# Performance work log

Measured on AMD Instinct MI355X. Metric: run time of the kernel, lower is better.

Reference implementation:

```python
import jax, jax.numpy as jnp
import numpy as np

N_WORDS, MAX_CHARS = 32768, 16
WORD_DIM, CHAR_DIM, HIDDEN = 256, 64, 256
VOCAB = 256


def setup_inputs() -> dict:
    key = jax.random.key(0)
    ks = jax.random.split(key, 10)
    char_indices = jax.random.randint(ks[0], (N_WORDS, MAX_CHARS), 0, VOCAB)
    char_lengths = jax.random.randint(ks[1], (N_WORDS,), 1, MAX_CHARS + 1)
    word_emb = jax.random.normal(ks[2], (N_WORDS, WORD_DIM), dtype=jnp.float32)
    s = 0.05
    E_char = jax.random.normal(ks[3], (VOCAB, CHAR_DIM), dtype=jnp.float32) * s
    W_ih = jax.random.normal(ks[4], (4 * HIDDEN, CHAR_DIM), dtype=jnp.float32) * s
    W_hh = jax.random.normal(ks[5], (4 * HIDDEN, HIDDEN), dtype=jnp.float32) * s
    b_ih = jax.random.normal(ks[6], (4 * HIDDEN,), dtype=jnp.float32) * s
    b_hh = jax.random.normal(ks[7], (4 * HIDDEN,), dtype=jnp.float32) * s
    W_lin = jax.random.normal(ks[8], (WORD_DIM, WORD_DIM + HIDDEN), dtype=jnp.float32) * s
    b_lin = jax.random.normal(ks[9], (WORD_DIM,), dtype=jnp.float32) * s
    return dict(char_indices=char_indices, char_lengths=char_lengths,
                word_emb=word_emb, E_char=E_char, W_ih=W_ih, W_hh=W_hh,
                b_ih=b_ih, b_hh=b_hh, W_lin=W_lin, b_lin=b_lin)


def _lstm_last_hidden(x, lengths, W_ih, W_hh, b_ih, b_hh):
    # x: [N, T, E]; returns final hidden h at position length-1 per row.
    N, T, _ = x.shape
    H = W_hh.shape[1]
    x_proj = jnp.einsum('nte,ge->ntg', x, W_ih) + (b_ih + b_hh)  # [N, T, 4H]
    x_proj = jnp.transpose(x_proj, (1, 0, 2))                    # time-major [T, N, 4H]

    def step(carry, inp):
        h, c = carry
        xg, t = inp
        gates = xg + h @ W_hh.T
        i, f, g, o = jnp.split(gates, 4, axis=-1)
        i, f, o = jax.nn.sigmoid(i), jax.nn.sigmoid(f), jax.nn.sigmoid(o)
        g = jnp.tanh(g)
        c_new = f * c + i * g
        h_new = o * jnp.tanh(c_new)
        mask = (t < lengths)[:, None]  # freeze state past each word's length
        h = jnp.where(mask, h_new, h)
        c = jnp.where(mask, c_new, c)
        return (h, c), None

    h0 = jnp.zeros((N, H), dtype=x.dtype)
    c0 = jnp.zeros((N, H), dtype=x.dtype)
    (h, _), _ = jax.lax.scan(step, (h0, c0), (x_proj, jnp.arange(T)))
    return h


def reference(char_indices, char_lengths, word_emb, E_char, W_ih, W_hh,
              b_ih, b_hh, W_lin, b_lin):
    char_embedded = E_char[char_indices]                        # [N, T, E]
    h = _lstm_last_hidden(char_embedded, char_lengths, W_ih, W_hh, b_ih, b_hh)
    combined = jnp.concatenate([word_emb, h], axis=-1)          # [N, WORD+H]
    return jax.nn.relu(combined @ W_lin.T + b_lin)              # [N, WORD]
```

## Files before the change

kernel.cpp:

```cpp
#include <hip/hip_runtime.h>


#define NW 32768

typedef __attribute__((ext_vector_type(8))) short short8;
typedef __attribute__((ext_vector_type(4))) float f32x4;
typedef __attribute__((ext_vector_type(4))) int i32x4;

#define MFMA16(a,b,c) __builtin_amdgcn_mfma_f32_16x16x32_bf16(a,b,c,0,0,0)
#define MFMAI8(a,b,c) __builtin_amdgcn_mfma_i32_16x16x32_i8(a,b,c,0,0,0)

#define O_ORDER 0
#define O_SLEN  131072
#define O_WPK   262144
#define O_USTP  589824
#define O_BIAS  593920
#define O_CHT   598016
#define O_WLIN  614400

__device__ inline unsigned short f2b(float f) {
  unsigned u = __builtin_bit_cast(unsigned, f);
  u = u + 0x7fffu + ((u >> 16) & 1u);
  return (unsigned short)(u >> 16);
}
__device__ inline float fsigm(float x) {
  float e = __builtin_amdgcn_exp2f(-1.44269504f * x);
  return __builtin_amdgcn_rcpf(1.0f + e);
}
__device__ inline float ftanh(float x) {
  float e = __builtin_amdgcn_exp2f(2.88539008f * x);
  return 1.0f - 2.0f * __builtin_amdgcn_rcpf(e + 1.0f);
}

__global__ void k_prep0(const float* __restrict__ wih, const float* __restrict__ whh,
                        const float* __restrict__ bih, const float* __restrict__ bhh,
                        const float* __restrict__ ech, unsigned char* __restrict__ ws) {
  int i = blockIdx.x * 256 + threadIdx.x;
  if (i < 1024) {
    float mx = 0.f;
    for (int k = 0; k < 64; ++k)  mx = fmaxf(mx, fabsf(wih[i * 64 + k]) * 0.25f);
    for (int k = 0; k < 256; ++k) mx = fmaxf(mx, fabsf(whh[i * 256 + k]));
    ((float*)(ws + O_USTP))[i] = mx / (127.f * 127.f);
    ((float*)(ws + O_BIAS))[i] = bih[i] + bhh[i];
    return;
  }
  int j = i - 1024;
  if (j < 16384) {
    float v = 508.f * ech[j];
    int q = (int)__builtin_rintf(v);
    q = q < -127 ? -127 : (q > 127 ? 127 : q);
    ((signed char*)(ws + O_CHT))[j] = (signed char)q;
  }
}

__global__ void k_prep1(const float* __restrict__ wih, const float* __restrict__ whh,
                        const float* __restrict__ wlin, unsigned char* __restrict__ ws) {
  int i = blockIdx.x * 256 + threadIdx.x;
  if (i < 327680) {
    int j = i & 7, lane = (i >> 3) & 63, t2 = i >> 9;
    int nt = t2 & 7, u2 = t2 >> 3;
    int kb = u2 % 10, w = u2 / 10;
    int n = (nt >> 1) * 256 + w * 32 + (nt & 1) * 16 + (lane & 15);
    int k = kb * 32 + (lane >> 4) * 8 + j;
    float v = (k < 64) ? wih[n * 64 + k] * 0.25f : whh[n * 256 + (k - 64)];
    float ustep = ((const float*)(ws + O_USTP))[n] * 127.f;
    float qf = (ustep > 0.f) ? v / ustep : 0.f;
    int q = (int)__builtin_rintf(qf);
    q = q < -127 ? -127 : (q > 127 ? 127 : q);
    ((signed char*)(ws + O_WPK))[i] = (signed char)q;
    return;
  }
  int i2 = i - 327680;
  if (i2 < 131072) {
    int j = i2 & 7, lane = (i2 >> 3) & 63, t3 = i2 >> 9;
    int kf = t3 & 15, nn = t3 >> 4;
    int n = (nn >> 2) * 64 + (nn & 3) * 16 + (lane & 15);
    int k = kf * 32 + (lane >> 4) * 8 + j;
    ((unsigned short*)(ws + O_WLIN))[i2] = f2b(wlin[n * 512 + k]);
  }
}

__global__ void k_sort(const int* __restrict__ lens, unsigned char* __restrict__ ws) {
  __shared__ unsigned hist[16], pos[16];
  int tid = threadIdx.x;
  if (tid < 16) hist[tid] = 0;
  __syncthreads();
  for (int w = tid; w < NW; w += 1024) {
    int l = lens[w]; l = l < 1 ? 1 : (l > 16 ? 16 : l);
    atomicAdd(&hist[l - 1], 1u);
  }
  __syncthreads();
  if (tid == 0) {
    unsigned acc = 0;
    for (int l = 0; l < 16; ++l) { pos[l] = acc; acc += hist[l]; }
  }
  __syncthreads();
  int* order = (int*)(ws + O_ORDER);
  int* slenp = (int*)(ws + O_SLEN);
  for (int w = tid; w < NW; w += 1024) {
    int l = lens[w]; l = l < 1 ? 1 : (l > 16 ? 16 : l);
    unsigned p = atomicAdd(&pos[l - 1], 1u);
    order[p] = w; slenp[p] = l;
  }
}

__global__ __launch_bounds__(512, 2) void k_main(
    const int* __restrict__ cidx, const float* __restrict__ wemb,
    const float* __restrict__ blin, float* __restrict__ outp,
    const unsigned char* __restrict__ ws) {
  extern __shared__ signed char smem[];
  signed char (*WL)[8][8][64][8] = (signed char (*)[8][8][64][8])smem;
  signed char (*Xb)[10][64][8] = (signed char (*)[10][64][8])(smem + 98304);
  signed char (*CT)[64] = (signed char (*)[64])(smem + 98304 + 20480);
  int (*CW)[16] = (int (*)[16])(smem + 98304 + 20480 + 16384);

  const int tid = threadIdx.x, b = blockIdx.x;
  const int w = tid >> 6, lane = tid & 63;
  const int q = lane >> 4, l15 = lane & 15;

  const int* order = (const int*)(ws + O_ORDER);
  const int* slen  = (const int*)(ws + O_SLEN);
  const signed char* wpk = (const signed char*)(ws + O_WPK);
  const float* upt = (const float*)(ws + O_USTP);
  const float* bsg = (const float*)(ws + O_BIAS);
  const unsigned short* wlin = (const unsigned short*)(ws + O_WLIN);

  {
    long* d = (long*)&CT[0][0];
    const long* s = (const long*)(ws + O_CHT);
    #pragma unroll
    for (int ii = 0; ii < 4; ++ii) d[tid + 512 * ii] = s[tid + 512 * ii];
  }
  long wreg[7][8];
  #pragma unroll
  for (int kb = 0; kb < 7; ++kb)
    #pragma unroll
    for (int nt = 0; nt < 8; ++nt)
      wreg[kb][nt] = *(const long*)(wpk + (((w * 10 + kb) * 8 + nt) * 64 + lane) * 8);
  #pragma unroll
  for (int c = 0; c < 24; ++c) {
    int kb = c >> 3, nt = c & 7;
    *(long*)&WL[kb][w][nt][lane][0] =
        *(const long*)(wpk + (((w * 10 + 7 + kb) * 8 + nt) * 64 + lane) * 8);
  }
  float uq[8], bq[8];
  #pragma unroll
  for (int nt = 0; nt < 8; ++nt) {
    int n = (nt >> 1) * 256 + w * 32 + (nt & 1) * 16 + l15;
    uq[nt] = upt[n]; bq[nt] = bsg[n];
  }
  const int mh = w >> 2, nw = w & 3;
  float blv[4];
  #pragma unroll
  for (int nt = 0; nt < 4; ++nt) blv[nt] = blin[nw * 64 + nt * 16 + l15];

  for (int sl = 0; sl < 2; ++sl) {
    const int s = sl ? (511 - b) : b;
    const int base = 64 * s;
    __syncthreads();

    {
      long* p = (long*)&Xb[0][0][0][0];
      #pragma unroll
      for (int ii = 0; ii < 4; ++ii) {
        int idx = tid + 512 * ii;
        int mt = idx >> 9, rem = idx & 511;
        p[mt * 640 + 128 + rem] = 0L;
      }
    }
    if (tid < 256) {
      int m = tid >> 2, part = tid & 3;
      int wid = order[base + m];
      *(i32x4*)&CW[m][part * 4] = *(const i32x4*)(cidx + wid * 16 + part * 4);
    }
    int tmax[4]; unsigned lenpk[4];
    #pragma unroll
    for (int mt = 0; mt < 4; ++mt) {
      int pbm = base + 16 * mt;
      tmax[mt] = slen[pbm + 15];
      unsigned l0 = (unsigned)slen[pbm + q * 4 + 0];
      unsigned l1 = (unsigned)slen[pbm + q * 4 + 1];
      unsigned l2 = (unsigned)slen[pbm + q * 4 + 2];
      unsigned l3 = (unsigned)slen[pbm + q * 4 + 3];
      lenpk[mt] = l0 | (l1 << 8) | (l2 << 16) | (l3 << 24);
    }
    const int Tm = tmax[3];
    __syncthreads();
    {
      int m = tid >> 3, c = tid & 7, kb = c >> 2, kq = c & 3;
      int ch = CW[m][0] & 255;
      *(long*)&Xb[m >> 4][kb][(m & 15) + 16 * kq][0] = *(const long*)&CT[ch][kb * 32 + kq * 8];
    }
    __syncthreads();

    float creg[4][2][4];
    #pragma unroll
    for (int mt = 0; mt < 4; ++mt)
      #pragma unroll
      for (int hs = 0; hs < 2; ++hs)
        #pragma unroll
        for (int r = 0; r < 4; ++r) creg[mt][hs][r] = 0.f;
    unsigned hpack[4][2];

    for (int t = 0; t < Tm; ++t) {
      bool actm[4];
      actm[0] = t < tmax[0]; actm[1] = t < tmax[1];
      actm[2] = t < tmax[2]; actm[3] = true;

      #pragma unroll
      for (int mt = 0; mt < 4; ++mt) {
        if (!actm[mt]) continue;
        i32x4 acc[8];
        #pragma unroll
        for (int nt = 0; nt < 8; ++nt) acc[nt] = (i32x4)0;
        #pragma unroll
        for (int kb = 0; kb < 7; ++kb) {
          long A = *(const long*)&Xb[mt][kb][lane][0];
          #pragma unroll
          for (int nt = 0; nt < 8; ++nt) acc[nt] = MFMAI8(A, wreg[kb][nt], acc[nt]);
        }
        #pragma unroll
        for (int kb = 7; kb < 10; ++kb) {
          long A = *(const long*)&Xb[mt][kb][lane][0];
          #pragma unroll
          for (int nt = 0; nt < 8; ++nt) {
            long Bv = *(const long*)&WL[kb - 7][w][nt][lane][0];
            acc[nt] = MFMAI8(A, Bv, acc[nt]);
          }
        }
        #pragma unroll
        for (int hs = 0; hs < 2; ++hs) {
          unsigned hp = 0;
          #pragma unroll
          for (int r = 0; r < 4; ++r) {
            float gi = (float)acc[0 + hs][r] * uq[0 + hs] + bq[0 + hs];
            float gf = (float)acc[2 + hs][r] * uq[2 + hs] + bq[2 + hs];
            float gg = (float)acc[4 + hs][r] * uq[4 + hs] + bq[4 + hs];
            float go = (float)acc[6 + hs][r] * uq[6 + hs] + bq[6 + hs];
            float si = fsigm(gi), sf = fsigm(gf);
            float sg = ftanh(gg), so = fsigm(go);
            float cold = creg[mt][hs][r];
            float cn = sf * cold + si * sg;
            float hn = so * ftanh(cn);
            int lene = (int)((lenpk[mt] >> (8 * r)) & 255u);
            creg[mt][hs][r] = (t < lene) ? cn : cold;
            int hq = (int)__builtin_rintf(127.f * hn);
            hq = hq < -127 ? -127 : (hq > 127 ? 127 : hq);
            hp |= ((unsigned)hq & 255u) << (8 * r);
          }
          hpack[mt][hs] = hp;
        }
      }
      __syncthreads();

      #pragma unroll
      for (int mt = 0; mt < 4; ++mt) {
        if (!actm[mt]) continue;
        #pragma unroll
        for (int hs = 0; hs < 2; ++hs) {
          int kqp = hs * 2 + (l15 >> 3);
          #pragma unroll
          for (int r = 0; r < 4; ++r) {
            int lene = (int)((lenpk[mt] >> (8 * r)) & 255u);
            if (t < lene)
              Xb[mt][2 + w][(q * 4 + r) + 16 * kqp][l15 & 7] =
                  (signed char)((hpack[mt][hs] >> (8 * r)) & 255u);
          }
        }
      }
      if (t + 1 < Tm) {
        int m = tid >> 3, c = tid & 7, kb = c >> 2, kq = c & 3;
        int ch = CW[m][t + 1] & 255;
        *(long*)&Xb[m >> 4][kb][(m & 15) + 16 * kq][0] = *(const long*)&CT[ch][kb * 32 + kq * 8];
      }
      __syncthreads();
    }

    int widA[2];
    #pragma unroll
    for (int mi = 0; mi < 2; ++mi) widA[mi] = order[base + (2 * mh + mi) * 16 + l15];
    f32x4 fac[2][4];
    #pragma unroll
    for (int mi = 0; mi < 2; ++mi)
      #pragma unroll
      for (int nt = 0; nt < 4; ++nt) fac[mi][nt] = 0.0f;

    #pragma unroll
    for (int kf = 0; kf < 16; ++kf) {
      short8 Bn[4];
      #pragma unroll
      for (int nt = 0; nt < 4; ++nt)
        Bn[nt] = ((const short8*)wlin)[((nw * 4 + nt) * 16 + kf) * 64 + lane];
      short8 Am[2];
      #pragma unroll
      for (int mi = 0; mi < 2; ++mi) {
        if (kf < 8) {
          const f32x4* pa = (const f32x4*)(wemb + widA[mi] * 256 + kf * 32 + q * 8);
          f32x4 f0 = pa[0], f1 = pa[1];
          short8 A;
          A[0] = (short)f2b(f0[0]); A[1] = (short)f2b(f0[1]);
          A[2] = (short)f2b(f0[2]); A[3] = (short)f2b(f0[3]);
          A[4] = (short)f2b(f1[0]); A[5] = (short)f2b(f1[1]);
          A[6] = (short)f2b(f1[2]); A[7] = (short)f2b(f1[3]);
          Am[mi] = A;
        } else {
          long ch = *(const long*)&Xb[2 * mh + mi][kf - 6][lane][0];
          short8 A;
          #pragma unroll
          for (int j = 0; j < 8; ++j) {
            int v = (int)(signed char)((ch >> (8 * j)) & 255);
            A[j] = (short)f2b((float)v * (1.f / 127.f));
          }
          Am[mi] = A;
        }
      }
      #pragma unroll
      for (int mi = 0; mi < 2; ++mi)
        #pragma unroll
        for (int nt = 0; nt < 4; ++nt)
          fac[mi][nt] = MFMA16(Am[mi], Bn[nt], fac[mi][nt]);
    }
    #pragma unroll
    for (int mi = 0; mi < 2; ++mi) {
      #pragma unroll
      for (int r = 0; r < 4; ++r) {
        int wid = order[base + (2 * mh + mi) * 16 + q * 4 + r];
        float* po = outp + wid * 256 + nw * 64 + l15;
        #pragma unroll
        for (int nt = 0; nt < 4; ++nt) {
          float v = fac[mi][nt][r] + blv[nt];
          po[nt * 16] = v > 0.f ? v : 0.f;
        }
      }
    }
  }
}

extern "C" void kernel_launch(void* const* d_in, const int* in_sizes, int n_in,
                              void* d_out, int out_size, void* d_ws, size_t ws_size,
                              hipStream_t stream) {
  const int*   cidx = (const int*)d_in[0];
  const int*   clen = (const int*)d_in[1];
  const float* wemb = (const float*)d_in[2];
  const float* ech  = (const float*)d_in[3];
  const float* wih  = (const float*)d_in[4];
  const float* whh  = (const float*)d_in[5];
  const float* bih  = (const float*)d_in[6];
  const float* bhh  = (const float*)d_in[7];
  const float* wlin = (const float*)d_in[8];
  const float* blin = (const float*)d_in[9];
  float* outp = (float*)d_out;
  unsigned char* ws = (unsigned char*)d_ws;

  k_prep0<<<68, 256, 0, stream>>>(wih, whh, bih, bhh, ech, ws);
  k_prep1<<<1792, 256, 0, stream>>>(wih, whh, wlin, ws);
  k_sort<<<1, 1024, 0, stream>>>(clen, ws);
  k_main<<<256, 512, 139264, stream>>>(cidx, wemb, blin, outp, ws);
}
```

Baseline: 449.7 us.

## Use 16x16x64 int8 MFMA, double-buffer LSTM state, and overlap MFMA with gate math

Measured after the change: 740.1 us. 1.65x slower.

```diff
diff --git a/kernel.cpp b/kernel.cpp
--- a/kernel.cpp
+++ b/kernel.cpp
@@ -7,8 +7,8 @@
 typedef __attribute__((ext_vector_type(4))) float f32x4;
 typedef __attribute__((ext_vector_type(4))) int i32x4;
 
-#define MFMA16(a,b,c) __builtin_amdgcn_mfma_f32_16x16x32_bf16(a,b,c,0,0,0)
-#define MFMAI8(a,b,c) __builtin_amdgcn_mfma_i32_16x16x32_i8(a,b,c,0,0,0)
+#define MFMA16(a,b,c)  __builtin_amdgcn_mfma_f32_16x16x32_bf16(a,b,c,0,0,0)
+#define MFMAI64(a,b,c) __builtin_amdgcn_mfma_i32_16x16x64_i8(a,b,c,0,0,0)
 
 #define O_ORDER 0
 #define O_SLEN  131072
@@ -23,45 +23,40 @@
   u = u + 0x7fffu + ((u >> 16) & 1u);
   return (unsigned short)(u >> 16);
 }
-__device__ inline float fsigm(float x) {
-  float e = __builtin_amdgcn_exp2f(-1.44269504f * x);
-  return __builtin_amdgcn_rcpf(1.0f + e);
-}
-__device__ inline float ftanh(float x) {
-  float e = __builtin_amdgcn_exp2f(2.88539008f * x);
-  return 1.0f - 2.0f * __builtin_amdgcn_rcpf(e + 1.0f);
-}
-
-__global__ void k_prep0(const float* __restrict__ wih, const float* __restrict__ whh,
+
+__global__ void k_prepA(const float* __restrict__ wih, const float* __restrict__ whh,
                         const float* __restrict__ bih, const float* __restrict__ bhh,
                         const float* __restrict__ ech, unsigned char* __restrict__ ws) {
-  int i = blockIdx.x * 256 + threadIdx.x;
-  if (i < 1024) {
-    float mx = 0.f;
-    for (int k = 0; k < 64; ++k)  mx = fmaxf(mx, fabsf(wih[i * 64 + k]) * 0.25f);
-    for (int k = 0; k < 256; ++k) mx = fmaxf(mx, fabsf(whh[i * 256 + k]));
-    ((float*)(ws + O_USTP))[i] = mx / (127.f * 127.f);
-    ((float*)(ws + O_BIAS))[i] = bih[i] + bhh[i];
+  int b = blockIdx.x, tid = threadIdx.x;
+  if (b < 256) {
+    int n = b * 4 + (tid >> 6), lane = tid & 63;
+    float m = fabsf(wih[n * 64 + lane]) * 0.25f;
+    #pragma unroll
+    for (int c = 0; c < 4; ++c) m = fmaxf(m, fabsf(whh[n * 256 + c * 64 + lane]));
+    #pragma unroll
+    for (int off = 32; off; off >>= 1) m = fmaxf(m, __shfl_xor(m, off));
+    if (lane == 0) {
+      ((float*)(ws + O_USTP))[n] = m / 16129.f;
+      ((float*)(ws + O_BIAS))[n] = bih[n] + bhh[n];
+    }
     return;
   }
-  int j = i - 1024;
-  if (j < 16384) {
-    float v = 508.f * ech[j];
-    int q = (int)__builtin_rintf(v);
-    q = q < -127 ? -127 : (q > 127 ? 127 : q);
-    ((signed char*)(ws + O_CHT))[j] = (signed char)q;
-  }
-}
-
-__global__ void k_prep1(const float* __restrict__ wih, const float* __restrict__ whh,
+  int idx = (b - 256) * 256 + tid;
+  int q = (int)__builtin_rintf(508.f * ech[idx]);
+  q = q < -127 ? -127 : (q > 127 ? 127 : q);
+  ((signed char*)(ws + O_CHT))[idx] = (signed char)q;
+}
+
+__global__ void k_prepB(const float* __restrict__ wih, const float* __restrict__ whh,
                         const float* __restrict__ wlin, unsigned char* __restrict__ ws) {
   int i = blockIdx.x * 256 + threadIdx.x;
   if (i < 327680) {
-    int j = i & 7, lane = (i >> 3) & 63, t2 = i >> 9;
-    int nt = t2 & 7, u2 = t2 >> 3;
-    int kb = u2 % 10, w = u2 / 10;
-    int n = (nt >> 1) * 256 + w * 32 + (nt & 1) * 16 + (lane & 15);
-    int k = kb * 32 + (lane >> 4) * 8 + j;
+    int j = i & 15, lane = (i >> 4) & 63, t = i >> 10;
+    int f = t & 7, u = t >> 3;
+    int kb = u % 5, w = u / 5;
+    int g = f >> 1, cc = f & 1;
+    int n = g * 256 + w * 32 + cc * 16 + (lane & 15);
+    int k = kb * 64 + (lane >> 4) * 16 + j;
     float v = (k < 64) ? wih[n * 64 + k] * 0.25f : whh[n * 256 + (k - 64)];
     float ustep = ((const float*)(ws + O_USTP))[n] * 127.f;
     float qf = (ustep > 0.f) ? v / ustep : 0.f;
@@ -71,13 +66,11 @@
     return;
   }
   int i2 = i - 327680;
-  if (i2 < 131072) {
-    int j = i2 & 7, lane = (i2 >> 3) & 63, t3 = i2 >> 9;
-    int kf = t3 & 15, nn = t3 >> 4;
-    int n = (nn >> 2) * 64 + (nn & 3) * 16 + (lane & 15);
-    int k = kf * 32 + (lane >> 4) * 8 + j;
-    ((unsigned short*)(ws + O_WLIN))[i2] = f2b(wlin[n * 512 + k]);
-  }
+  int j = i2 & 7, lane = (i2 >> 3) & 63, t3 = i2 >> 9;
+  int kf = t3 & 15, nn = t3 >> 4;
+  int n = (nn >> 2) * 64 + (nn & 3) * 16 + (lane & 15);
+  int k = kf * 32 + (lane >> 4) * 8 + j;
+  ((unsigned short*)(ws + O_WLIN))[i2] = f2b(wlin[n * 512 + k]);
 }
 
 __global__ void k_sort(const int* __restrict__ lens, unsigned char* __restrict__ ws) {
@@ -104,15 +97,19 @@
   }
 }
 
+#define L_WL 40960
+#define L_CT 106496
+#define L_CW 122880
+
 __global__ __launch_bounds__(512, 2) void k_main(
     const int* __restrict__ cidx, const float* __restrict__ wemb,
     const float* __restrict__ blin, float* __restrict__ outp,
     const unsigned char* __restrict__ ws) {
-  extern __shared__ signed char smem[];
-  signed char (*WL)[8][8][64][8] = (signed char (*)[8][8][64][8])smem;
-  signed char (*Xb)[10][64][8] = (signed char (*)[10][64][8])(smem + 98304);
-  signed char (*CT)[64] = (signed char (*)[64])(smem + 98304 + 20480);
-  int (*CW)[16] = (int (*)[16])(smem + 98304 + 20480 + 16384);
+  extern __shared__ unsigned char smem[];
+  signed char (*Xb)[4][5][64][16] = (signed char (*)[4][5][64][16])smem;
+  signed char (*WL)[8][64][16]    = (signed char (*)[8][64][16])(smem + L_WL);
+  signed char (*CT)[64]           = (signed char (*)[64])(smem + L_CT);
+  int (*CW)[16]                   = (int (*)[16])(smem + L_CW);
 
   const int tid = threadIdx.x, b = blockIdx.x;
   const int w = tid >> 6, lane = tid & 63;
@@ -121,34 +118,29 @@
   const int* order = (const int*)(ws + O_ORDER);
   const int* slen  = (const int*)(ws + O_SLEN);
   const signed char* wpk = (const signed char*)(ws + O_WPK);
-  const float* upt = (const float*)(ws + O_USTP);
-  const float* bsg = (const float*)(ws + O_BIAS);
   const unsigned short* wlin = (const unsigned short*)(ws + O_WLIN);
 
-  {
-    long* d = (long*)&CT[0][0];
-    const long* s = (const long*)(ws + O_CHT);
-    #pragma unroll
-    for (int ii = 0; ii < 4; ++ii) d[tid + 512 * ii] = s[tid + 512 * ii];
-  }
-  long wreg[7][8];
+  ((i32x4*)CT)[tid]       = ((const i32x4*)(ws + O_CHT))[tid];
+  ((i32x4*)CT)[512 + tid] = ((const i32x4*)(ws + O_CHT))[512 + tid];
+  i32x4 wreg[4][8];
   #pragma unroll
-  for (int kb = 0; kb < 7; ++kb)
-    #pragma unroll
-    for (int nt = 0; nt < 8; ++nt)
-      wreg[kb][nt] = *(const long*)(wpk + (((w * 10 + kb) * 8 + nt) * 64 + lane) * 8);
+  for (int kb = 0; kb < 4; ++kb)
+    #pragma unroll
+    for (int f = 0; f < 8; ++f)
+      wreg[kb][f] = *(const i32x4*)(wpk + (((w * 5 + kb) * 8 + f) * 64 + lane) * 16);
   #pragma unroll
-  for (int c = 0; c < 24; ++c) {
-    int kb = c >> 3, nt = c & 7;
-    *(long*)&WL[kb][w][nt][lane][0] =
-        *(const long*)(wpk + (((w * 10 + 7 + kb) * 8 + nt) * 64 + lane) * 8);
-  }
-  float uq[8], bq[8];
+  for (int f = 0; f < 8; ++f)
+    *(i32x4*)&WL[w][f][lane][0] =
+        *(const i32x4*)(wpk + (((w * 5 + 4) * 8 + f) * 64 + lane) * 16);
+  float uq[2][4], bq[2][4];
   #pragma unroll
-  for (int nt = 0; nt < 8; ++nt) {
-    int n = (nt >> 1) * 256 + w * 32 + (nt & 1) * 16 + l15;
-    uq[nt] = upt[n]; bq[nt] = bsg[n];
-  }
+  for (int cc = 0; cc < 2; ++cc)
+    #pragma unroll
+    for (int g = 0; g < 4; ++g) {
+      int n = g * 256 + w * 32 + cc * 16 + l15;
+      uq[cc][g] = ((const float*)(ws + O_USTP))[n];
+      bq[cc][g] = ((const float*)(ws + O_BIAS))[n];
+    }
   const int mh = w >> 2, nw = w & 3;
   float blv[4];
   #pragma unroll
@@ -160,12 +152,11 @@
     __syncthreads();
 
     {
-      long* p = (long*)&Xb[0][0][0][0];
-      #pragma unroll
-      for (int ii = 0; ii < 4; ++ii) {
+      #pragma unroll
+      for (int ii = 0; ii < 2; ++ii) {
         int idx = tid + 512 * ii;
-        int mt = idx >> 9, rem = idx & 511;
-        p[mt * 640 + 128 + rem] = 0L;
+        int mt = idx >> 8, off = idx & 255;
+        *(i32x4*)(&Xb[0][mt][1][0][0] + off * 16) = (i32x4)0;
       }
     }
     if (tid < 256) {
@@ -173,109 +164,108 @@
       int wid = order[base + m];
       *(i32x4*)&CW[m][part * 4] = *(const i32x4*)(cidx + wid * 16 + part * 4);
     }
-    int tmax[4]; unsigned lenpk[4];
+    unsigned lenpk[4];
     #pragma unroll
     for (int mt = 0; mt < 4; ++mt) {
       int pbm = base + 16 * mt;
-      tmax[mt] = slen[pbm + 15];
       unsigned l0 = (unsigned)slen[pbm + q * 4 + 0];
       unsigned l1 = (unsigned)slen[pbm + q * 4 + 1];
       unsigned l2 = (unsigned)slen[pbm + q * 4 + 2];
       unsigned l3 = (unsigned)slen[pbm + q * 4 + 3];
       lenpk[mt] = l0 | (l1 << 8) | (l2 << 16) | (l3 << 24);
     }
-    const int Tm = tmax[3];
+    const int Tm = slen[base + 63];
     __syncthreads();
-    {
-      int m = tid >> 3, c = tid & 7, kb = c >> 2, kq = c & 3;
+    if (tid < 256) {
+      int m = tid >> 2, c = tid & 3;
       int ch = CW[m][0] & 255;
-      *(long*)&Xb[m >> 4][kb][(m & 15) + 16 * kq][0] = *(const long*)&CT[ch][kb * 32 + kq * 8];
+      *(i32x4*)&Xb[0][m >> 4][0][(m & 15) + 16 * c][0] = *(const i32x4*)&CT[ch][c * 16];
     }
     __syncthreads();
 
-    float creg[4][2][4];
+    f32x4 creg[4][2];
     #pragma unroll
     for (int mt = 0; mt < 4; ++mt)
       #pragma unroll
-      for (int hs = 0; hs < 2; ++hs)
-        #pragma unroll
-        for (int r = 0; r < 4; ++r) creg[mt][hs][r] = 0.f;
-    unsigned hpack[4][2];
+      for (int cc = 0; cc < 2; ++cc) creg[mt][cc] = 0.0f;
+    unsigned fhold[4][2] = {};
 
     for (int t = 0; t < Tm; ++t) {
-      bool actm[4];
-      actm[0] = t < tmax[0]; actm[1] = t < tmax[1];
-      actm[2] = t < tmax[2]; actm[3] = true;
-
-      #pragma unroll
-      for (int mt = 0; mt < 4; ++mt) {
-        if (!actm[mt]) continue;
-        i32x4 acc[8];
-        #pragma unroll
-        for (int nt = 0; nt < 8; ++nt) acc[nt] = (i32x4)0;
-        #pragma unroll
-        for (int kb = 0; kb < 7; ++kb) {
-          long A = *(const long*)&Xb[mt][kb][lane][0];
-          #pragma unroll
-          for (int nt = 0; nt < 8; ++nt) acc[nt] = MFMAI8(A, wreg[kb][nt], acc[nt]);
-        }
-        #pragma unroll
-        for (int kb = 7; kb < 10; ++kb) {
-          long A = *(const long*)&Xb[mt][kb][lane][0];
-          #pragma unroll
-          for (int nt = 0; nt < 8; ++nt) {
-            long Bv = *(const long*)&WL[kb - 7][w][nt][lane][0];
-            acc[nt] = MFMAI8(A, Bv, acc[nt]);
+      const int cur = t & 1, nxt = cur ^ 1;
+      i32x4 acc0[4], acc1[4];
+
+      auto stage_mfma = [&](int mt, int cc, i32x4* acc) {
+        #pragma unroll
+        for (int g = 0; g < 4; ++g) acc[g] = (i32x4)0;
+        #pragma unroll
+        for (int kb = 0; kb < 5; ++kb) {
+          i32x4 A = *(const i32x4*)&Xb[cur][mt][kb][lane][0];
+          if (kb < 4) {
+            #pragma unroll
+            for (int g = 0; g < 4; ++g)
+              acc[g] = MFMAI64(A, wreg[kb][g * 2 + cc], acc[g]);
+          } else {
+            #pragma unroll
+            for (int g = 0; g < 4; ++g) {
+              i32x4 Bv = *(const i32x4*)&WL[w][g * 2 + cc][lane][0];
+              acc[g] = MFMAI64(A, Bv, acc[g]);
+            }
           }
         }
-        #pragma unroll
-        for (int hs = 0; hs < 2; ++hs) {
-          unsigned hp = 0;
-          #pragma unroll
-          for (int r = 0; r < 4; ++r) {
-            float gi = (float)acc[0 + hs][r] * uq[0 + hs] + bq[0 + hs];
-            float gf = (float)acc[2 + hs][r] * uq[2 + hs] + bq[2 + hs];
-            float gg = (float)acc[4 + hs][r] * uq[4 + hs] + bq[4 + hs];
-            float go = (float)acc[6 + hs][r] * uq[6 + hs] + bq[6 + hs];
-            float si = fsigm(gi), sf = fsigm(gf);
-            float sg = ftanh(gg), so = fsigm(go);
-            float cold = creg[mt][hs][r];
-            float cn = sf * cold + si * sg;
-            float hn = so * ftanh(cn);
-            int lene = (int)((lenpk[mt] >> (8 * r)) & 255u);
-            creg[mt][hs][r] = (t < lene) ? cn : cold;
-            int hq = (int)__builtin_rintf(127.f * hn);
-            hq = hq < -127 ? -127 : (hq > 127 ? 127 : hq);
-            hp |= ((unsigned)hq & 255u) << (8 * r);
-          }
-          hpack[mt][hs] = hp;
+      };
+      auto stage_update = [&](int mt, int cc, i32x4* acc) {
+        const int kbh = 1 + ((w * 2 + cc) >> 2);
+        const int sub = (4 + w * 2 + cc) & 3;
+        unsigned fh = fhold[mt][cc], newf = 0;
+        #pragma unroll
+        for (int r = 0; r < 4; ++r) {
+          float gi = (float)acc[0][r] * uq[cc][0] + bq[cc][0];
+          float gf = (float)acc[1][r] * uq[cc][1] + bq[cc][1];
+          float gg = (float)acc[2][r] * uq[cc][2] + bq[cc][2];
+          float go = (float)acc[3][r] * uq[cc][3] + bq[cc][3];
+          gi = fminf(30.f, fmaxf(-30.f, gi));
+          gf = fminf(30.f, fmaxf(-30.f, gf));
+          gg = fminf(30.f, fmaxf(-30.f, gg));
+          go = fminf(30.f, fmaxf(-30.f, go));
+          float ei  = __builtin_amdgcn_exp2f(-1.44269504f * gi);
+          float ef  = __builtin_amdgcn_exp2f(-1.44269504f * gf);
+          float eg2 = __builtin_amdgcn_exp2f( 2.88539008f * gg);
+          float eo  = __builtin_amdgcn_exp2f(-1.44269504f * go);
+          float cold = creg[mt][cc][r];
+          float cn = cold * __builtin_amdgcn_rcpf(1.f + ef) +
+                     (eg2 - 1.f) * __builtin_amdgcn_rcpf((1.f + ei) * (1.f + eg2));
+          float ec = __builtin_amdgcn_exp2f(2.88539008f * cn);
+          float hn = (ec - 1.f) * __builtin_amdgcn_rcpf((1.f + eo) * (ec + 1.f));
+          int lene = (int)((lenpk[mt] >> (8 * r)) & 255u);
+          bool act = t < lene;
+          creg[mt][cc][r] = act ? cn : cold;
+          int hq = (int)__builtin_rintf(127.f * hn);
+          hq = hq < -127 ? -127 : (hq > 127 ? 127 : hq);
+          unsigned ob = act ? ((unsigned)hq & 255u) : ((fh >> (8 * r)) & 255u);
+          newf |= ob << (8 * r);
+          if (t <= lene)
+            Xb[nxt][mt][kbh][(q * 4 + r) + 16 * sub][l15] = (signed char)ob;
         }
+        fhold[mt][cc] = newf;
+      };
+
+      stage_mfma(0, 0, acc0);
+      #pragma unroll
+      for (int s2 = 0; s2 < 8; ++s2) {
+        i32x4* curA = (s2 & 1) ? acc1 : acc0;
+        i32x4* nxtA = (s2 & 1) ? acc0 : acc1;
+        if (s2 < 7) stage_mfma((s2 + 1) >> 1, (s2 + 1) & 1, nxtA);
+        stage_update(s2 >> 1, s2 & 1, curA);
+      }
+      if (t + 1 < Tm && tid < 256) {
+        int m = tid >> 2, c = tid & 3;
+        int ch = CW[m][t + 1] & 255;
+        *(i32x4*)&Xb[nxt][m >> 4][0][(m & 15) + 16 * c][0] = *(const i32x4*)&CT[ch][c * 16];
       }
       __syncthreads();
-
-      #pragma unroll
-      for (int mt = 0; mt < 4; ++mt) {
-        if (!actm[mt]) continue;
-        #pragma unroll
-        for (int hs = 0; hs < 2; ++hs) {
-          int kqp = hs * 2 + (l15 >> 3);
-          #pragma unroll
-          for (int r = 0; r < 4; ++r) {
-            int lene = (int)((lenpk[mt] >> (8 * r)) & 255u);
-            if (t < lene)
-              Xb[mt][2 + w][(q * 4 + r) + 16 * kqp][l15 & 7] =
-                  (signed char)((hpack[mt][hs] >> (8 * r)) & 255u);
-          }
-        }
-      }
-      if (t + 1 < Tm) {
-        int m = tid >> 3, c = tid & 7, kb = c >> 2, kq = c & 3;
-        int ch = CW[m][t + 1] & 255;
-        *(long*)&Xb[m >> 4][kb][(m & 15) + 16 * kq][0] = *(const long*)&CT[ch][kb * 32 + kq * 8];
-      }
-      __syncthreads();
-    }
-
+    }
+
+    const int e = Tm & 1;
     int widA[2];
     #pragma unroll
     for (int mi = 0; mi < 2; ++mi) widA[mi] = order[base + (2 * mh + mi) * 16 + l15];
@@ -304,7 +294,9 @@
           A[6] = (short)f2b(f1[2]); A[7] = (short)f2b(f1[3]);
           Am[mi] = A;
         } else {
-          long ch = *(const long*)&Xb[2 * mh + mi][kf - 6][lane][0];
+          int K0 = 64 + (kf - 8) * 32 + q * 8;
+          long ch = *(const long*)&Xb[e][2 * mh + mi][K0 >> 6]
+                                     [l15 + 16 * ((K0 >> 4) & 3)][K0 & 15];
           short8 A;
           #pragma unroll
           for (int j = 0; j < 8; ++j) {
@@ -352,8 +344,8 @@
   float* outp = (float*)d_out;
   unsigned char* ws = (unsigned char*)d_ws;
 
-  k_prep0<<<68, 256, 0, stream>>>(wih, whh, bih, bhh, ech, ws);
-  k_prep1<<<1792, 256, 0, stream>>>(wih, whh, wlin, ws);
+  k_prepA<<<320, 256, 0, stream>>>(wih, whh, bih, bhh, ech, ws);
+  k_prepB<<<1792, 256, 0, stream>>>(wih, whh, wlin, ws);
   k_sort<<<1, 1024, 0, stream>>>(clen, ws);
-  k_main<<<256, 512, 139264, stream>>>(cidx, wemb, blin, outp, ws);
-}
+  k_main<<<256, 512, 126976, stream>>>(cidx, wemb, blin, outp, ws);
+}
```
